# Performance work log

Hardware: AMD Instinct MI355X
Metric: run time of the kernel (lower is better)

## Reference

```python
import jax, jax.numpy as jnp
import numpy as np

N = 1_000_000
D = 128
P = 16384  # number of person segments


def setup_inputs() -> dict:
    key = jax.random.key(0)
    k1, k2, k3, k4, k5 = jax.random.split(key, 5)
    x = jax.random.normal(k1, (N, D), dtype=jnp.float32)
    person_ids = jnp.sort(jax.random.randint(k2, (N,), 0, P, dtype=jnp.int32))
    dh = D // 4
    # attention MLP params: Linear(D, D//4) -> tanh -> Linear(D//4, 1)
    W1 = jax.random.normal(k3, (D, dh), dtype=jnp.float32) / np.sqrt(D)
    b1 = jnp.zeros((dh,), dtype=jnp.float32)
    W2 = jax.random.normal(k4, (dh, 1), dtype=jnp.float32) / np.sqrt(dh)
    b2 = jnp.zeros((1,), dtype=jnp.float32)
    return {"x": x, "person_ids": person_ids, "W1": W1, "b1": b1, "W2": W2, "b2": b2}


def reference(x, person_ids, W1, b1, W2, b2):
    # attention scores per node: (N,)
    scores = (jnp.tanh(x @ W1 + b1) @ W2 + b2).squeeze(-1)
    # per-segment numerically-stable softmax (one fused O(N) pass)
    seg_max = jax.ops.segment_max(scores, person_ids, num_segments=P)
    seg_max = jnp.where(jnp.isfinite(seg_max), seg_max, 0.0)  # guard empty segments
    e = jnp.exp(scores - seg_max[person_ids])
    denom = jax.ops.segment_sum(e, person_ids, num_segments=P)
    denom = jnp.where(denom == 0.0, 1.0, denom)
    w = e / denom[person_ids]                     # (N,)
    pooled = jax.ops.segment_sum(w[:, None] * x, person_ids, num_segments=P)  # (P, D)
    pooled_pids = jnp.arange(P, dtype=person_ids.dtype)
    return pooled, pooled_pids
```

## Files before the change

kernel.cpp:

```cpp
#include <hip/hip_runtime.h>

#define D_  128
#define DH_ 32

typedef __attribute__((ext_vector_type(8))) short bf16x8;
typedef __attribute__((ext_vector_type(4))) float f32x4;

__device__ __forceinline__ short f2bf(float f) {
    unsigned u = __float_as_uint(f);
    unsigned r = (u + 0x7FFF + ((u >> 16) & 1)) >> 16;
    return (short)r;
}

__global__ __launch_bounds__(256, 4) void tap_main(
    const float* __restrict__ x,
    const int*   __restrict__ pid,
    const float* __restrict__ W1,
    const float* __restrict__ b1,
    const float* __restrict__ W2,
    const float* __restrict__ b2,
    float* __restrict__ out,
    int N, int P)
{
    __shared__ int   sid[256];
    __shared__ float se[256];

    const int tid  = threadIdx.x;
    const int lane = tid & 63;
    const int wave = tid >> 6;
    const int row0 = blockIdx.x * 256;
    const int rb   = wave * 64;

    { int gr = row0 + tid; if (gr > N - 1) gr = N - 1; sid[tid] = pid[gr]; }

    const int n16  = lane & 15;
    const int quad = lane >> 4;

    bf16x8 bfrag[4][2];
    #pragma unroll
    for (int kt = 0; kt < 4; ++kt)
        #pragma unroll
        for (int jt = 0; jt < 2; ++jt) {
            const float* wp = W1 + (kt * 32 + quad * 8) * DH_ + jt * 16 + n16;
            #pragma unroll
            for (int i = 0; i < 8; ++i) bfrag[kt][jt][i] = f2bf(wp[i * DH_]);
        }

    f32x4 acc[4][2] = {};

    for (int kt = 0; kt < 4; ++kt) {
        bf16x8 afrag[4];
        #pragma unroll
        for (int mt = 0; mt < 4; ++mt) {
            int r = row0 + rb + mt * 16 + n16; if (r > N - 1) r = N - 1;
            const float* ap = x + (size_t)r * D_ + kt * 32 + quad * 8;
            float4 v0 = *(const float4*)ap;
            float4 v1 = *(const float4*)(ap + 4);
            afrag[mt][0] = f2bf(v0.x); afrag[mt][1] = f2bf(v0.y);
            afrag[mt][2] = f2bf(v0.z); afrag[mt][3] = f2bf(v0.w);
            afrag[mt][4] = f2bf(v1.x); afrag[mt][5] = f2bf(v1.y);
            afrag[mt][6] = f2bf(v1.z); afrag[mt][7] = f2bf(v1.w);
        }
        #pragma unroll
        for (int mt = 0; mt < 4; ++mt)
            #pragma unroll
            for (int jt = 0; jt < 2; ++jt)
                acc[mt][jt] = __builtin_amdgcn_mfma_f32_16x16x32_bf16(
                    afrag[mt], bfrag[kt][jt], acc[mt][jt], 0, 0, 0);
    }

    const float b2v = b2[0];
    float w2v[2], b1v[2];
    #pragma unroll
    for (int jt = 0; jt < 2; ++jt) {
        w2v[jt] = W2[jt * 16 + n16];
        b1v[jt] = b1[jt * 16 + n16];
    }

    #pragma unroll
    for (int mt = 0; mt < 4; ++mt) {
        #pragma unroll
        for (int q = 0; q < 4; ++q) {
            float s = 0.f;
            #pragma unroll
            for (int jt = 0; jt < 2; ++jt) {
                float h = acc[mt][jt][q] + b1v[jt];
                h = fminf(fmaxf(h, -15.f), 15.f);
                float z = __expf(2.f * h);
                float t = 1.f - 2.f / (z + 1.f);
                s = fmaf(t, w2v[jt], s);
            }
            s += __shfl_xor(s, 1);
            s += __shfl_xor(s, 2);
            s += __shfl_xor(s, 4);
            s += __shfl_xor(s, 8);
            if (n16 == 0) {
                int rloc = rb + mt * 16 + quad * 4 + q;
                int gr   = row0 + rloc;
                se[rloc] = (gr < N) ? __expf(s + b2v) : 0.f;
            }
        }
    }

    float a0 = 0.f, a1 = 0.f, ad = 0.f;
    int   cur = sid[rb];
    #pragma unroll
    for (int r = rb; r < rb + 64; ++r) {
        int sg = sid[r];
        if (sg != cur) {
            atomicAdd(&out[cur * D_ + 2 * lane],     a0);
            atomicAdd(&out[cur * D_ + 2 * lane + 1], a1);
            if (lane == 0) atomicAdd(&out[P * D_ + cur], ad);
            a0 = a1 = ad = 0.f;
            cur = sg;
        }
        float ev = se[r];
        int gr = row0 + r; if (gr > N - 1) gr = N - 1;
        const float2 xv = *(const float2*)&x[(size_t)gr * D_ + 2 * lane];
        a0 = fmaf(ev, xv.x, a0);
        a1 = fmaf(ev, xv.y, a1);
        ad += ev;
    }
    atomicAdd(&out[cur * D_ + 2 * lane],     a0);
    atomicAdd(&out[cur * D_ + 2 * lane + 1], a1);
    if (lane == 0) atomicAdd(&out[P * D_ + cur], ad);
}

__global__ __launch_bounds__(128) void tap_finalize(float* __restrict__ out, int P)
{
    const int p = blockIdx.x;
    const int f = threadIdx.x;
    float den = out[P * D_ + p];
    den = (den == 0.f) ? 1.f : den;
    float v = out[p * D_ + f];
    __syncthreads();
    out[p * D_ + f] = v / den;
    if (f == 0) out[P * D_ + p] = (float)p;
}

extern "C" void kernel_launch(void* const* d_in, const int* in_sizes, int n_in,
                              void* d_out, int out_size, void* d_ws, size_t ws_size,
                              hipStream_t stream)
{
    const float* x   = (const float*)d_in[0];
    const int*   pid = (const int*)d_in[1];
    const float* W1  = (const float*)d_in[2];
    const float* b1  = (const float*)d_in[3];
    const float* W2  = (const float*)d_in[4];
    const float* b2  = (const float*)d_in[5];
    float* out = (float*)d_out;

    const int N = in_sizes[0] / D_;
    const int P = out_size / (D_ + 1);

    hipMemsetAsync(d_out, 0, (size_t)out_size * sizeof(float), stream);

    const int blocks = (N + 255) / 256;
    tap_main<<<blocks, 256, 0, stream>>>(x, pid, W1, b1, W2, b2, out, N, P);
    tap_finalize<<<P, 128, 0, stream>>>(out, P);
}
```

Measured before the change: 749.1 us.

## Stage x rows in swizzled LDS via direct global-to-LDS loads, reuse for pooling

Each block now covers 128 rows with 8 waves of 16 rows. Every x row is copied once into a swizzled 64KB LDS tile using global_load_lds, and both the MFMA score pass and the weighted pooling pass read from that tile. Before, the pooling pass re-read x from global memory. Segment ids and exp scores now travel through wave shuffles instead of shared arrays. The large LDS footprint limits how many blocks fit per CU, and each wave now has less MFMA work to hide latency.

```diff
diff --git a/kernel.cpp b/kernel.cpp
--- a/kernel.cpp
+++ b/kernel.cpp
@@ -12,7 +12,14 @@
     return (short)r;
 }
 
-__global__ __launch_bounds__(256, 4) void tap_main(
+typedef __attribute__((address_space(1))) const void gvoid_t;
+typedef __attribute__((address_space(3))) void svoid_t;
+
+__device__ __forceinline__ void gload_lds16(const float* g, float* l) {
+    __builtin_amdgcn_global_load_lds((gvoid_t*)g, (svoid_t*)l, 16, 0, 0);
+}
+
+__global__ __launch_bounds__(512, 4) void tap_main(
     const float* __restrict__ x,
     const int*   __restrict__ pid,
     const float* __restrict__ W1,
@@ -22,19 +29,33 @@
     float* __restrict__ out,
     int N, int P)
 {
-    __shared__ int   sid[256];
-    __shared__ float se[256];
+    __shared__ float xs[128 * D_];
 
     const int tid  = threadIdx.x;
     const int lane = tid & 63;
     const int wave = tid >> 6;
-    const int row0 = blockIdx.x * 256;
-    const int rb   = wave * 64;
-
-    { int gr = row0 + tid; if (gr > N - 1) gr = N - 1; sid[tid] = pid[gr]; }
+    const int lb   = wave * 16;
+    const int row0 = blockIdx.x * 128;
+    const int R0   = row0 + lb;
 
     const int n16  = lane & 15;
     const int quad = lane >> 4;
+
+    {
+        const int slot = lane & 31;
+        const int half = lane >> 5;
+        #pragma unroll
+        for (int t = 0; t < 8; ++t) {
+            int lr = lb + t * 2 + half;
+            int gr = R0 + t * 2 + half; if (gr > N - 1) gr = N - 1;
+            unsigned sb = ((unsigned)(slot * 16)) ^ ((unsigned)((lr & 31) << 4));
+            gload_lds16(x + (size_t)gr * D_ + (sb >> 2),
+                        xs + (size_t)(lb + t * 2) * D_);
+        }
+    }
+
+    int pr;
+    { int gr = R0 + n16; if (gr > N - 1) gr = N - 1; pr = pid[gr]; }
 
     bf16x8 bfrag[4][2];
     #pragma unroll
@@ -46,27 +67,27 @@
             for (int i = 0; i < 8; ++i) bfrag[kt][jt][i] = f2bf(wp[i * DH_]);
         }
 
-    f32x4 acc[4][2] = {};
+    f32x4 acc[2] = {};
 
+    asm volatile("s_waitcnt vmcnt(0)" ::: "memory");
+
+    const int lr_a = lb + n16;
+    const unsigned swz_a = (unsigned)((lr_a & 31) << 4);
+    const char* xrow = (const char*)xs + (size_t)lr_a * (D_ * 4);
+    #pragma unroll
     for (int kt = 0; kt < 4; ++kt) {
-        bf16x8 afrag[4];
+        unsigned b0 = (unsigned)(kt * 128 + quad * 32);
+        float4 v0 = *(const float4*)(xrow + (b0 ^ swz_a));
+        float4 v1 = *(const float4*)(xrow + ((b0 + 16) ^ swz_a));
+        bf16x8 af;
+        af[0] = f2bf(v0.x); af[1] = f2bf(v0.y);
+        af[2] = f2bf(v0.z); af[3] = f2bf(v0.w);
+        af[4] = f2bf(v1.x); af[5] = f2bf(v1.y);
+        af[6] = f2bf(v1.z); af[7] = f2bf(v1.w);
         #pragma unroll
-        for (int mt = 0; mt < 4; ++mt) {
-            int r = row0 + rb + mt * 16 + n16; if (r > N - 1) r = N - 1;
-            const float* ap = x + (size_t)r * D_ + kt * 32 + quad * 8;
-            float4 v0 = *(const float4*)ap;
-            float4 v1 = *(const float4*)(ap + 4);
-            afrag[mt][0] = f2bf(v0.x); afrag[mt][1] = f2bf(v0.y);
-            afrag[mt][2] = f2bf(v0.z); afrag[mt][3] = f2bf(v0.w);
-            afrag[mt][4] = f2bf(v1.x); afrag[mt][5] = f2bf(v1.y);
-            afrag[mt][6] = f2bf(v1.z); afrag[mt][7] = f2bf(v1.w);
-        }
-        #pragma unroll
-        for (int mt = 0; mt < 4; ++mt)
-            #pragma unroll
-            for (int jt = 0; jt < 2; ++jt)
-                acc[mt][jt] = __builtin_amdgcn_mfma_f32_16x16x32_bf16(
-                    afrag[mt], bfrag[kt][jt], acc[mt][jt], 0, 0, 0);
+        for (int jt = 0; jt < 2; ++jt)
+            acc[jt] = __builtin_amdgcn_mfma_f32_16x16x32_bf16(
+                af, bfrag[kt][jt], acc[jt], 0, 0, 0);
     }
 
     const float b2v = b2[0];
@@ -77,36 +98,31 @@
         b1v[jt] = b1[jt * 16 + n16];
     }
 
+    float e[4];
     #pragma unroll
-    for (int mt = 0; mt < 4; ++mt) {
+    for (int q = 0; q < 4; ++q) {
+        float s = 0.f;
         #pragma unroll
-        for (int q = 0; q < 4; ++q) {
-            float s = 0.f;
-            #pragma unroll
-            for (int jt = 0; jt < 2; ++jt) {
-                float h = acc[mt][jt][q] + b1v[jt];
-                h = fminf(fmaxf(h, -15.f), 15.f);
-                float z = __expf(2.f * h);
-                float t = 1.f - 2.f / (z + 1.f);
-                s = fmaf(t, w2v[jt], s);
-            }
-            s += __shfl_xor(s, 1);
-            s += __shfl_xor(s, 2);
-            s += __shfl_xor(s, 4);
-            s += __shfl_xor(s, 8);
-            if (n16 == 0) {
-                int rloc = rb + mt * 16 + quad * 4 + q;
-                int gr   = row0 + rloc;
-                se[rloc] = (gr < N) ? __expf(s + b2v) : 0.f;
-            }
+        for (int jt = 0; jt < 2; ++jt) {
+            float h = acc[jt][q] + b1v[jt];
+            h = fminf(fmaxf(h, -15.f), 15.f);
+            float z = __expf(2.f * h);
+            float t = 1.f - 2.f / (z + 1.f);
+            s = fmaf(t, w2v[jt], s);
         }
+        s += __shfl_xor(s, 1);
+        s += __shfl_xor(s, 2);
+        s += __shfl_xor(s, 4);
+        s += __shfl_xor(s, 8);
+        int gr = R0 + quad * 4 + q;
+        e[q] = (gr < N) ? __expf(s + b2v) : 0.f;
     }
 
     float a0 = 0.f, a1 = 0.f, ad = 0.f;
-    int   cur = sid[rb];
+    int   cur = __shfl(pr, 0);
     #pragma unroll
-    for (int r = rb; r < rb + 64; ++r) {
-        int sg = sid[r];
+    for (int r = 0; r < 16; ++r) {
+        int sg = __shfl(pr, r);
         if (sg != cur) {
             atomicAdd(&out[cur * D_ + 2 * lane],     a0);
             atomicAdd(&out[cur * D_ + 2 * lane + 1], a1);
@@ -114,9 +130,11 @@
             a0 = a1 = ad = 0.f;
             cur = sg;
         }
-        float ev = se[r];
-        int gr = row0 + r; if (gr > N - 1) gr = N - 1;
-        const float2 xv = *(const float2*)&x[(size_t)gr * D_ + 2 * lane];
+        float ev = __shfl(e[r & 3], (r >> 2) << 4);
+        int lr = lb + r;
+        unsigned swz = (unsigned)((lr & 31) << 4);
+        const float2 xv = *(const float2*)(
+            (const char*)xs + (size_t)lr * (D_ * 4) + (((unsigned)(lane * 8)) ^ swz));
         a0 = fmaf(ev, xv.x, a0);
         a1 = fmaf(ev, xv.y, a1);
         ad += ev;
@@ -155,7 +173,7 @@
 
     hipMemsetAsync(d_out, 0, (size_t)out_size * sizeof(float), stream);
 
-    const int blocks = (N + 255) / 256;
-    tap_main<<<blocks, 256, 0, stream>>>(x, pid, W1, b1, W2, b2, out, N, P);
+    const int blocks = (N + 127) / 128;
+    tap_main<<<blocks, 512, 0, stream>>>(x, pid, W1, b1, W2, b2, out, N, P);
     tap_finalize<<<P, 128, 0, stream>>>(out, P);
 }
```

Result: faster. 689.3 us (-8.0%).
